# Kernel tuning notes

Measured on AMD Instinct MI355X. Metric: run time of the kernel, lower is better.

## Reference

```python
import jax, jax.numpy as jnp
import numpy as np

N_NODES = 100000


def setup_inputs() -> dict:
    key = jax.random.key(0)
    ks = jax.random.split(key, 6)
    d_in, d_hid, d_out = 128, 128, 128
    x = jax.random.normal(ks[0], (N_NODES, d_in), dtype=jnp.float32)
    # edge_index[0] = row (destination), edge_index[1] = col (source)
    edge_index = jax.random.randint(ks[1], (2, 1000000), 0, N_NODES, dtype=jnp.int64)
    W1 = jax.random.normal(ks[2], (2 * d_in, d_hid), dtype=jnp.float32) * (1.0 / np.sqrt(2 * d_in))
    b1 = jnp.zeros((d_hid,), dtype=jnp.float32)
    W2 = jax.random.normal(ks[3], (2 * d_hid, d_out), dtype=jnp.float32) * (1.0 / np.sqrt(2 * d_hid))
    b2 = jnp.zeros((d_out,), dtype=jnp.float32)
    return {"x": x, "edge_index": edge_index, "W1": W1, "b1": b1, "W2": W2, "b2": b2}


def _mean_aggregate(x, row, col, inv_deg):
    # out[i] = (1/deg(i)) * sum_{(i,j) in E} x[j]   (cogdl MeanAggregator: row_norm + spmm)
    agg = jax.ops.segment_sum(x[col], row, num_segments=x.shape[0])  # [N, d]
    return agg * inv_deg[:, None]


def _sage_layer(x, row, col, inv_deg, W, b):
    agg = _mean_aggregate(x, row, col, inv_deg)
    h = jnp.concatenate([x, agg], axis=-1)  # [N, 2d]
    return h @ W + b


def reference(x, edge_index, W1, b1, W2, b2):
    row, col = edge_index[0], edge_index[1]
    n = x.shape[0]
    deg = jax.ops.segment_sum(jnp.ones(row.shape, dtype=x.dtype), row, num_segments=n)
    inv_deg = jnp.where(deg > 0, 1.0 / jnp.maximum(deg, 1.0), 0.0).astype(x.dtype)
    h = jax.nn.relu(_sage_layer(x, row, col, inv_deg, W1, b1))
    # (dropout omitted: deterministic/eval reference)
    out = _sage_layer(h, row, col, inv_deg, W2, b2)
    return out
```

## Files before the change

### kernel.cpp

```cpp
#include <hip/hip_runtime.h>

#define D 128
#define MAXDEG 64
#define BIN_SHIFT 7
#define BINCAP 2048
#define EPB 8192

typedef short short8 __attribute__((ext_vector_type(8)));
typedef short short4v __attribute__((ext_vector_type(4)));
typedef float float4v __attribute__((ext_vector_type(4)));

__device__ __forceinline__ unsigned short f2bf(float f) {
    union { float f; unsigned u; } v; v.f = f;
    unsigned r = v.u + 0x7FFFu + ((v.u >> 16) & 1u);
    return (unsigned short)(r >> 16);
}
__device__ __forceinline__ float bflo(unsigned p) {
    union { unsigned u; float f; } v; v.u = p << 16; return v.f;
}
__device__ __forceinline__ float bfhi(unsigned p) {
    union { unsigned u; float f; } v; v.u = p & 0xFFFF0000u; return v.f;
}

__global__ __launch_bounds__(1024) void bin_kernel(const int* __restrict__ row,
                                                   const int* __restrict__ col,
                                                   int* __restrict__ bincnt,
                                                   long long* __restrict__ binbuf,
                                                   int nE, int nbins) {
    __shared__ int bcnt[1024];
    __shared__ int bbase[1024];
    const int t = threadIdx.x;
    const int e0 = blockIdx.x * EPB + t * 8;
    if (t < nbins) bcnt[t] = 0;
    __syncthreads();

    int rr[8], cc[8], bin[8], pos[8];
    if (e0 + 8 <= nE) {
        int4 r0 = *(const int4*)&row[e0];
        int4 r1 = *(const int4*)&row[e0 + 4];
        int4 c0 = *(const int4*)&col[e0];
        int4 c1 = *(const int4*)&col[e0 + 4];
        rr[0] = r0.x; rr[1] = r0.y; rr[2] = r0.z; rr[3] = r0.w;
        rr[4] = r1.x; rr[5] = r1.y; rr[6] = r1.z; rr[7] = r1.w;
        cc[0] = c0.x; cc[1] = c0.y; cc[2] = c0.z; cc[3] = c0.w;
        cc[4] = c1.x; cc[5] = c1.y; cc[6] = c1.z; cc[7] = c1.w;
        #pragma unroll
        for (int k = 0; k < 8; ++k) {
            bin[k] = rr[k] >> BIN_SHIFT;
            pos[k] = atomicAdd(&bcnt[bin[k]], 1);
        }
    } else {
        #pragma unroll
        for (int k = 0; k < 8; ++k) {
            int e = e0 + k;
            if (e < nE) {
                rr[k] = row[e]; cc[k] = col[e];
                bin[k] = rr[k] >> BIN_SHIFT;
                pos[k] = atomicAdd(&bcnt[bin[k]], 1);
            } else { pos[k] = -1; bin[k] = 0; rr[k] = 0; cc[k] = 0; }
        }
    }
    __syncthreads();

    if (t < nbins) {
        int c = bcnt[t];
        bbase[t] = (c > 0) ? atomicAdd(&bincnt[t << 4], c) : 0;
    }
    __syncthreads();

    #pragma unroll
    for (int k = 0; k < 8; ++k) {
        if (pos[k] >= 0) {
            int slot = bbase[bin[k]] + pos[k];
            if (slot < BINCAP)
                binbuf[(size_t)bin[k] * BINCAP + slot] =
                    ((long long)cc[k] << 32) | (unsigned)rr[k];
        }
    }
}

__global__ __launch_bounds__(256) void ellbuild_kernel(const long long* __restrict__ binbuf,
                                                       const int* __restrict__ bincnt,
                                                       int* __restrict__ cnt,
                                                       int* __restrict__ bucket, int n) {
    __shared__ int lcnt[1 << BIN_SHIFT];
    const int b = blockIdx.x, t = threadIdx.x;
    const int base = b << BIN_SHIFT;
    if (t < (1 << BIN_SHIFT)) lcnt[t] = 0;
    __syncthreads();
    int m = bincnt[b << 4];
    if (m > BINCAP) m = BINCAP;
    const long long* buf = binbuf + (size_t)b * BINCAP;
    for (int j = t; j < m; j += 256) {
        long long pk = buf[j];
        int r = (int)pk;
        int c = (int)(pk >> 32);
        int pos = atomicAdd(&lcnt[r - base], 1);
        if (pos < MAXDEG) bucket[((size_t)r << 6) + pos] = c;
    }
    __syncthreads();
    if (t < (1 << BIN_SHIFT)) {
        int node = base + t;
        if (node < n) {
            int c0 = lcnt[t];
            cnt[node] = c0;
            int c = c0 > MAXDEG ? MAXDEG : c0;
            int cp = (c + 15) & ~15;
            for (int s = c; s < cp; ++s) bucket[((size_t)node << 6) + s] = n;
        }
    }
}

__global__ void conv_kernel(const float2* __restrict__ x, unsigned* __restrict__ xb, int nPairs,
                            const float* __restrict__ W1, const float* __restrict__ W2,
                            unsigned short* __restrict__ Wt1, unsigned short* __restrict__ Wt2,
                            unsigned* __restrict__ hb, int n) {
    int id = blockIdx.x * blockDim.x + threadIdx.x;
    if (blockIdx.x < 256) {
        int e = id & 32767;
        int c = e >> 8, k = e & 255;
        if (id < 32768) Wt1[c * 256 + k] = f2bf(W1[k * 128 + c]);
        else            Wt2[c * 256 + k] = f2bf(W2[k * 128 + c]);
    } else {
        if (blockIdx.x == 256 && threadIdx.x < 64) {
            xb[((size_t)n << 6) + threadIdx.x] = 0;
            hb[((size_t)n << 6) + threadIdx.x] = 0;
        }
        int stride = (gridDim.x - 256) * blockDim.x;
        for (int i = id - 65536; i < nPairs; i += stride) {
            float2 v = x[i];
            xb[i] = (unsigned)f2bf(v.x) | ((unsigned)f2bf(v.y) << 16);
        }
    }
}

__device__ __forceinline__ void gather16(const unsigned* __restrict__ feat,
                                         const int* __restrict__ bk, int j, unsigned lane,
                                         float& x0, float& x1, float& x2, float& x3,
                                         float& y0, float& y1, float& y2, float& y3) {
    int4 c0 = *(const int4*)&bk[j];
    int4 c1 = *(const int4*)&bk[j + 4];
    int4 c2 = *(const int4*)&bk[j + 8];
    int4 c3 = *(const int4*)&bk[j + 12];
    unsigned v0  = feat[((unsigned)c0.x << 6) + lane];
    unsigned v1  = feat[((unsigned)c0.y << 6) + lane];
    unsigned v2  = feat[((unsigned)c0.z << 6) + lane];
    unsigned v3  = feat[((unsigned)c0.w << 6) + lane];
    unsigned v4  = feat[((unsigned)c1.x << 6) + lane];
    unsigned v5  = feat[((unsigned)c1.y << 6) + lane];
    unsigned v6  = feat[((unsigned)c1.z << 6) + lane];
    unsigned v7  = feat[((unsigned)c1.w << 6) + lane];
    unsigned v8  = feat[((unsigned)c2.x << 6) + lane];
    unsigned v9  = feat[((unsigned)c2.y << 6) + lane];
    unsigned v10 = feat[((unsigned)c2.z << 6) + lane];
    unsigned v11 = feat[((unsigned)c2.w << 6) + lane];
    unsigned v12 = feat[((unsigned)c3.x << 6) + lane];
    unsigned v13 = feat[((unsigned)c3.y << 6) + lane];
    unsigned v14 = feat[((unsigned)c3.z << 6) + lane];
    unsigned v15 = feat[((unsigned)c3.w << 6) + lane];
    x0 += bflo(v0);  y0 += bfhi(v0);
    x1 += bflo(v1);  y1 += bfhi(v1);
    x2 += bflo(v2);  y2 += bfhi(v2);
    x3 += bflo(v3);  y3 += bfhi(v3);
    x0 += bflo(v4);  y0 += bfhi(v4);
    x1 += bflo(v5);  y1 += bfhi(v5);
    x2 += bflo(v6);  y2 += bfhi(v6);
    x3 += bflo(v7);  y3 += bfhi(v7);
    x0 += bflo(v8);  y0 += bfhi(v8);
    x1 += bflo(v9);  y1 += bfhi(v9);
    x2 += bflo(v10); y2 += bfhi(v10);
    x3 += bflo(v11); y3 += bfhi(v11);
    x0 += bflo(v12); y0 += bfhi(v12);
    x1 += bflo(v13); y1 += bfhi(v13);
    x2 += bflo(v14); y2 += bfhi(v14);
    x3 += bflo(v15); y3 += bfhi(v15);
}

__global__ __launch_bounds__(256) void agg_bf16_kernel(const unsigned* __restrict__ feat,
                                                       const int* __restrict__ cnt,
                                                       const int* __restrict__ bucket,
                                                       unsigned* __restrict__ agg, int n) {
    long long tid = (long long)blockIdx.x * blockDim.x + threadIdx.x;
    int w = (int)(tid >> 6);
    int iA = w * 2, iB = w * 2 + 1;
    if (iA >= n) return;
    const unsigned lane = (unsigned)tid & 63u;

    int dtA = cnt[iA];
    int dA = dtA > MAXDEG ? MAXDEG : dtA;
    int dpA = (dA + 15) & ~15;
    int dtB = 0, dpB = 0;
    if (iB < n) {
        dtB = cnt[iB];
        int dB = dtB > MAXDEG ? MAXDEG : dtB;
        dpB = (dB + 15) & ~15;
    }
    const int* bkA = bucket + ((size_t)iA << 6);
    const int* bkB = bucket + ((size_t)iB << 6);

    float ax0=0,ax1=0,ax2=0,ax3=0, ay0=0,ay1=0,ay2=0,ay3=0;
    float bx0=0,bx1=0,bx2=0,bx3=0, by0=0,by1=0,by2=0,by3=0;
    int jm = dpA > dpB ? dpA : dpB;
    for (int j = 0; j < jm; j += 16) {
        if (j < dpA) gather16(feat, bkA, j, lane, ax0,ax1,ax2,ax3, ay0,ay1,ay2,ay3);
        if (j < dpB) gather16(feat, bkB, j, lane, bx0,bx1,bx2,bx3, by0,by1,by2,by3);
    }

    float invA = (dtA > 0) ? 1.0f / (float)dtA : 0.0f;
    float rxA = ((ax0 + ax1) + (ax2 + ax3)) * invA;
    float ryA = ((ay0 + ay1) + (ay2 + ay3)) * invA;
    agg[((size_t)iA << 6) + lane] = (unsigned)f2bf(rxA) | ((unsigned)f2bf(ryA) << 16);
    if (iB < n) {
        float invB = (dtB > 0) ? 1.0f / (float)dtB : 0.0f;
        float rxB = ((bx0 + bx1) + (bx2 + bx3)) * invB;
        float ryB = ((by0 + by1) + (by2 + by3)) * invB;
        agg[((size_t)iB << 6) + lane] = (unsigned)f2bf(rxB) | ((unsigned)f2bf(ryB) << 16);
    }
}

template <bool RELU, bool OUTF32>
__global__ __launch_bounds__(256) void sage_mfma(const unsigned short* __restrict__ selfb,
                                                 const unsigned short* __restrict__ aggb,
                                                 const unsigned short* __restrict__ Wtb,
                                                 const float* __restrict__ bias,
                                                 float* __restrict__ outf,
                                                 unsigned short* __restrict__ outb,
                                                 int n) {
    __shared__ short Alds[64 * 256];
    const int tid  = threadIdx.x;
    const int wave = tid >> 6;
    const int lane = tid & 63;
    const int r15  = lane & 15, g = lane >> 4;
    const int rowbase = blockIdx.x * 64;

    #pragma unroll
    for (int it = 0; it < 8; ++it) {
        int id  = it * 256 + tid;
        int row = id >> 5, cin = id & 31;
        int rowG = rowbase + row; if (rowG >= n) rowG = n - 1;
        const unsigned short* src = (cin < 16)
            ? selfb + (size_t)rowG * D + cin * 8
            : aggb  + (size_t)rowG * D + (cin - 16) * 8;
        int dchunk = cin ^ (row & 7);
        *(short8*)&Alds[row * 256 + dchunk * 8] = *(const short8*)src;
    }

    const int colbase = wave * 32;
    short8 bfr[2][8];
    #pragma unroll
    for (int cf = 0; cf < 2; ++cf) {
        const unsigned short* wp = Wtb + (size_t)(colbase + cf * 16 + r15) * 256;
        #pragma unroll
        for (int ks = 0; ks < 8; ++ks) {
            short4v lo = *(const short4v*)(wp + ks * 32 + 4 * g);
            short4v hi = *(const short4v*)(wp + ks * 32 + 16 + 4 * g);
            bfr[cf][ks] = __builtin_shufflevector(lo, hi, 0, 1, 2, 3, 4, 5, 6, 7);
        }
    }
    float bv0 = bias[colbase + r15];
    float bv1 = bias[colbase + 16 + r15];
    float4v acc[4][2];
    #pragma unroll
    for (int rf = 0; rf < 4; ++rf) {
        acc[rf][0] = (float4v){bv0, bv0, bv0, bv0};
        acc[rf][1] = (float4v){bv1, bv1, bv1, bv1};
    }

    __syncthreads();

    const int sw = (r15 & 7) << 4;
    #pragma unroll
    for (int ks = 0; ks < 8; ++ks) {
        #pragma unroll
        for (int rf = 0; rf < 4; ++rf) {
            const char* pr = (const char*)&Alds[(rf * 16 + r15) * 256];
            short4v lo = *(const short4v*)(pr + ((ks * 64 + 8 * g) ^ sw));
            short4v hi = *(const short4v*)(pr + ((ks * 64 + 8 * g + 32) ^ sw));
            short8 af = __builtin_shufflevector(lo, hi, 0, 1, 2, 3, 4, 5, 6, 7);
            acc[rf][0] = __builtin_amdgcn_mfma_f32_16x16x32_bf16(af, bfr[0][ks], acc[rf][0], 0, 0, 0);
            acc[rf][1] = __builtin_amdgcn_mfma_f32_16x16x32_bf16(af, bfr[1][ks], acc[rf][1], 0, 0, 0);
        }
    }

    #pragma unroll
    for (int rf = 0; rf < 4; ++rf) {
        #pragma unroll
        for (int cf = 0; cf < 2; ++cf) {
            #pragma unroll
            for (int r = 0; r < 4; ++r) {
                int row = rowbase + rf * 16 + g * 4 + r;
                int col = colbase + cf * 16 + r15;
                if (row < n) {
                    float v = acc[rf][cf][r];
                    if (RELU) v = (v > 0.0f) ? v : 0.0f;
                    if (OUTF32) outf[(size_t)row * D + col] = v;
                    else        outb[(size_t)row * D + col] = f2bf(v);
                }
            }
        }
    }
}

extern "C" void kernel_launch(void* const* d_in, const int* in_sizes, int n_in,
                              void* d_out, int out_size, void* d_ws, size_t ws_size,
                              hipStream_t stream) {
    const float* x  = (const float*)d_in[0];
    const int*   ei = (const int*)d_in[1];
    const float* W1 = (const float*)d_in[2];
    const float* b1 = (const float*)d_in[3];
    const float* W2 = (const float*)d_in[4];
    const float* b2 = (const float*)d_in[5];
    float* out = (float*)d_out;

    const int n  = in_sizes[0] / D;
    const int nE = in_sizes[1] / 2;
    const int* row = ei;
    const int* col = ei + nE;
    const int nbins = (n + (1 << BIN_SHIFT) - 1) >> BIN_SHIFT;

    auto aup = [](size_t v) { return (v + 63) & ~(size_t)63; };
    int* wsI = (int*)d_ws;
    size_t o = 0;
    int* cnt    = wsI + o; o = aup(o + (size_t)n);
    int* bucket = wsI + o; o = aup(o + ((size_t)n << 6));
    unsigned* xb   = (unsigned*)(wsI + o); o = aup(o + (size_t)(n + 1) * 64);
    unsigned* hb   = (unsigned*)(wsI + o); o = aup(o + (size_t)(n + 1) * 64);
    unsigned* aggb = (unsigned*)(wsI + o); o = aup(o + (size_t)n * 64);
    unsigned short* Wt1 = (unsigned short*)(wsI + o); o = aup(o + 16384);
    unsigned short* Wt2 = (unsigned short*)(wsI + o); o = aup(o + 16384);
    int* bincnt = wsI + o; o = aup(o + (size_t)nbins * 16);
    long long* binbuf = (long long*)aggb;

    const int B = 256;
    const int binGrid = (nE + EPB - 1) / EPB;
    const int aggGrid = (int)((((long long)(n + 1) / 2) * 64 + B - 1) / B);
    const int mmGrid  = (n + 63) / 64;

    hipMemsetAsync(bincnt, 0, (size_t)nbins * 16 * sizeof(int), stream);
    bin_kernel<<<binGrid, 1024, 0, stream>>>(row, col, bincnt, binbuf, nE, nbins);
    ellbuild_kernel<<<nbins, B, 0, stream>>>(binbuf, bincnt, cnt, bucket, n);

    conv_kernel<<<2048 + 256, B, 0, stream>>>((const float2*)x, xb, n * 64,
                                              W1, W2, Wt1, Wt2, hb, n);

    agg_bf16_kernel<<<aggGrid, B, 0, stream>>>(xb, cnt, bucket, aggb, n);
    sage_mfma<true, false><<<mmGrid, B, 0, stream>>>(
        (const unsigned short*)xb, (const unsigned short*)aggb, Wt1, b1,
        nullptr, (unsigned short*)hb, n);

    agg_bf16_kernel<<<aggGrid, B, 0, stream>>>(hb, cnt, bucket, aggb, n);
    sage_mfma<false, true><<<mmGrid, B, 0, stream>>>(
        (const unsigned short*)hb, (const unsigned short*)aggb, Wt2, b2,
        out, nullptr, n);
}
```

Measured before the change: 200.8 us.

## Merge binning and conversion kernels; shrink GEMM row tile and stream weight fragments

Folds the edge-binning kernel and the bf16 conversion/weight-transpose kernel into one launch, with block ranges assigned to each task, to save a launch and let the two independent phases overlap. The MFMA linear-layer kernel now handles 32 rows per block instead of 64, which halves LDS use and doubles the block count. It also double-buffers B fragments from global memory per k-step instead of preloading all of them into registers. Per-block weight reloads grow, and the smaller tile gives less reuse of each weight fragment.

```diff
diff --git a/kernel.cpp b/kernel.cpp
--- a/kernel.cpp
+++ b/kernel.cpp
@@ -22,59 +22,87 @@
     union { unsigned u; float f; } v; v.u = p & 0xFFFF0000u; return v.f;
 }
 
-__global__ __launch_bounds__(1024) void bin_kernel(const int* __restrict__ row,
-                                                   const int* __restrict__ col,
-                                                   int* __restrict__ bincnt,
-                                                   long long* __restrict__ binbuf,
-                                                   int nE, int nbins) {
+__global__ __launch_bounds__(1024) void prep_kernel(const int* __restrict__ row,
+                                                    const int* __restrict__ col,
+                                                    int* __restrict__ bincnt,
+                                                    long long* __restrict__ binbuf,
+                                                    int nE, int nbins, int binGrid,
+                                                    const float2* __restrict__ x,
+                                                    unsigned* __restrict__ xb, int nPairs,
+                                                    const float* __restrict__ W1,
+                                                    const float* __restrict__ W2,
+                                                    unsigned short* __restrict__ Wt1,
+                                                    unsigned short* __restrict__ Wt2,
+                                                    unsigned* __restrict__ hb, int n) {
     __shared__ int bcnt[1024];
     __shared__ int bbase[1024];
     const int t = threadIdx.x;
-    const int e0 = blockIdx.x * EPB + t * 8;
-    if (t < nbins) bcnt[t] = 0;
-    __syncthreads();
-
-    int rr[8], cc[8], bin[8], pos[8];
-    if (e0 + 8 <= nE) {
-        int4 r0 = *(const int4*)&row[e0];
-        int4 r1 = *(const int4*)&row[e0 + 4];
-        int4 c0 = *(const int4*)&col[e0];
-        int4 c1 = *(const int4*)&col[e0 + 4];
-        rr[0] = r0.x; rr[1] = r0.y; rr[2] = r0.z; rr[3] = r0.w;
-        rr[4] = r1.x; rr[5] = r1.y; rr[6] = r1.z; rr[7] = r1.w;
-        cc[0] = c0.x; cc[1] = c0.y; cc[2] = c0.z; cc[3] = c0.w;
-        cc[4] = c1.x; cc[5] = c1.y; cc[6] = c1.z; cc[7] = c1.w;
+
+    if (blockIdx.x < (unsigned)binGrid) {
+        const int e0 = blockIdx.x * EPB + t * 8;
+        if (t < nbins) bcnt[t] = 0;
+        __syncthreads();
+
+        int rr[8], cc[8], bin[8], pos[8];
+        if (e0 + 8 <= nE) {
+            int4 r0 = *(const int4*)&row[e0];
+            int4 r1 = *(const int4*)&row[e0 + 4];
+            int4 c0 = *(const int4*)&col[e0];
+            int4 c1 = *(const int4*)&col[e0 + 4];
+            rr[0] = r0.x; rr[1] = r0.y; rr[2] = r0.z; rr[3] = r0.w;
+            rr[4] = r1.x; rr[5] = r1.y; rr[6] = r1.z; rr[7] = r1.w;
+            cc[0] = c0.x; cc[1] = c0.y; cc[2] = c0.z; cc[3] = c0.w;
+            cc[4] = c1.x; cc[5] = c1.y; cc[6] = c1.z; cc[7] = c1.w;
+            #pragma unroll
+            for (int k = 0; k < 8; ++k) {
+                bin[k] = rr[k] >> BIN_SHIFT;
+                pos[k] = atomicAdd(&bcnt[bin[k]], 1);
+            }
+        } else {
+            #pragma unroll
+            for (int k = 0; k < 8; ++k) {
+                int e = e0 + k;
+                if (e < nE) {
+                    rr[k] = row[e]; cc[k] = col[e];
+                    bin[k] = rr[k] >> BIN_SHIFT;
+                    pos[k] = atomicAdd(&bcnt[bin[k]], 1);
+                } else { pos[k] = -1; bin[k] = 0; rr[k] = 0; cc[k] = 0; }
+            }
+        }
+        __syncthreads();
+
+        if (t < nbins) {
+            int c = bcnt[t];
+            bbase[t] = (c > 0) ? atomicAdd(&bincnt[t << 4], c) : 0;
+        }
+        __syncthreads();
+
         #pragma unroll
         for (int k = 0; k < 8; ++k) {
-            bin[k] = rr[k] >> BIN_SHIFT;
-            pos[k] = atomicAdd(&bcnt[bin[k]], 1);
-        }
+            if (pos[k] >= 0) {
+                int slot = bbase[bin[k]] + pos[k];
+                if (slot < BINCAP)
+                    binbuf[(size_t)bin[k] * BINCAP + slot] =
+                        ((long long)cc[k] << 32) | (unsigned)rr[k];
+            }
+        }
+    } else if (blockIdx.x < (unsigned)(binGrid + 64)) {
+        int id = (blockIdx.x - binGrid) * 1024 + t;
+        int e = id & 32767;
+        int c = e >> 8, k = e & 255;
+        if (id < 32768) Wt1[c * 256 + k] = f2bf(W1[k * 128 + c]);
+        else            Wt2[c * 256 + k] = f2bf(W2[k * 128 + c]);
     } else {
-        #pragma unroll
-        for (int k = 0; k < 8; ++k) {
-            int e = e0 + k;
-            if (e < nE) {
-                rr[k] = row[e]; cc[k] = col[e];
-                bin[k] = rr[k] >> BIN_SHIFT;
-                pos[k] = atomicAdd(&bcnt[bin[k]], 1);
-            } else { pos[k] = -1; bin[k] = 0; rr[k] = 0; cc[k] = 0; }
-        }
-    }
-    __syncthreads();
-
-    if (t < nbins) {
-        int c = bcnt[t];
-        bbase[t] = (c > 0) ? atomicAdd(&bincnt[t << 4], c) : 0;
-    }
-    __syncthreads();
-
-    #pragma unroll
-    for (int k = 0; k < 8; ++k) {
-        if (pos[k] >= 0) {
-            int slot = bbase[bin[k]] + pos[k];
-            if (slot < BINCAP)
-                binbuf[(size_t)bin[k] * BINCAP + slot] =
-                    ((long long)cc[k] << 32) | (unsigned)rr[k];
+        int cb = blockIdx.x - binGrid - 64;
+        if (cb == 0 && t < 64) {
+            xb[((size_t)n << 6) + t] = 0;
+            hb[((size_t)n << 6) + t] = 0;
+        }
+        int id = cb * 1024 + t;
+        int stride = (gridDim.x - binGrid - 64) * 1024;
+        for (int i = id; i < nPairs; i += stride) {
+            float2 v = x[i];
+            xb[i] = (unsigned)f2bf(v.x) | ((unsigned)f2bf(v.y) << 16);
         }
     }
 }
@@ -107,29 +135,6 @@
             int c = c0 > MAXDEG ? MAXDEG : c0;
             int cp = (c + 15) & ~15;
             for (int s = c; s < cp; ++s) bucket[((size_t)node << 6) + s] = n;
-        }
-    }
-}
-
-__global__ void conv_kernel(const float2* __restrict__ x, unsigned* __restrict__ xb, int nPairs,
-                            const float* __restrict__ W1, const float* __restrict__ W2,
-                            unsigned short* __restrict__ Wt1, unsigned short* __restrict__ Wt2,
-                            unsigned* __restrict__ hb, int n) {
-    int id = blockIdx.x * blockDim.x + threadIdx.x;
-    if (blockIdx.x < 256) {
-        int e = id & 32767;
-        int c = e >> 8, k = e & 255;
-        if (id < 32768) Wt1[c * 256 + k] = f2bf(W1[k * 128 + c]);
-        else            Wt2[c * 256 + k] = f2bf(W2[k * 128 + c]);
-    } else {
-        if (blockIdx.x == 256 && threadIdx.x < 64) {
-            xb[((size_t)n << 6) + threadIdx.x] = 0;
-            hb[((size_t)n << 6) + threadIdx.x] = 0;
-        }
-        int stride = (gridDim.x - 256) * blockDim.x;
-        for (int i = id - 65536; i < nPairs; i += stride) {
-            float2 v = x[i];
-            xb[i] = (unsigned)f2bf(v.x) | ((unsigned)f2bf(v.y) << 16);
         }
     }
 }
@@ -218,6 +223,12 @@
     }
 }
 
+__device__ __forceinline__ short8 loadB(const unsigned short* __restrict__ wp, int ks, int g) {
+    short4v lo = *(const short4v*)(wp + ks * 32 + 4 * g);
+    short4v hi = *(const short4v*)(wp + ks * 32 + 16 + 4 * g);
+    return __builtin_shufflevector(lo, hi, 0, 1, 2, 3, 4, 5, 6, 7);
+}
+
 template <bool RELU, bool OUTF32>
 __global__ __launch_bounds__(256) void sage_mfma(const unsigned short* __restrict__ selfb,
                                                  const unsigned short* __restrict__ aggb,
@@ -226,15 +237,15 @@
                                                  float* __restrict__ outf,
                                                  unsigned short* __restrict__ outb,
                                                  int n) {
-    __shared__ short Alds[64 * 256];
+    __shared__ short Alds[32 * 256];
     const int tid  = threadIdx.x;
     const int wave = tid >> 6;
     const int lane = tid & 63;
     const int r15  = lane & 15, g = lane >> 4;
-    const int rowbase = blockIdx.x * 64;
+    const int rowbase = blockIdx.x * 32;
 
     #pragma unroll
-    for (int it = 0; it < 8; ++it) {
+    for (int it = 0; it < 4; ++it) {
         int id  = it * 256 + tid;
         int row = id >> 5, cin = id & 31;
         int rowG = rowbase + row; if (rowG >= n) rowG = n - 1;
@@ -246,44 +257,45 @@
     }
 
     const int colbase = wave * 32;
-    short8 bfr[2][8];
-    #pragma unroll
-    for (int cf = 0; cf < 2; ++cf) {
-        const unsigned short* wp = Wtb + (size_t)(colbase + cf * 16 + r15) * 256;
-        #pragma unroll
-        for (int ks = 0; ks < 8; ++ks) {
-            short4v lo = *(const short4v*)(wp + ks * 32 + 4 * g);
-            short4v hi = *(const short4v*)(wp + ks * 32 + 16 + 4 * g);
-            bfr[cf][ks] = __builtin_shufflevector(lo, hi, 0, 1, 2, 3, 4, 5, 6, 7);
-        }
-    }
+    const unsigned short* wp0 = Wtb + (size_t)(colbase + r15) * 256;
+    const unsigned short* wp1 = Wtb + (size_t)(colbase + 16 + r15) * 256;
     float bv0 = bias[colbase + r15];
     float bv1 = bias[colbase + 16 + r15];
-    float4v acc[4][2];
+    float4v acc[2][2];
     #pragma unroll
-    for (int rf = 0; rf < 4; ++rf) {
+    for (int rf = 0; rf < 2; ++rf) {
         acc[rf][0] = (float4v){bv0, bv0, bv0, bv0};
         acc[rf][1] = (float4v){bv1, bv1, bv1, bv1};
     }
+
+    short8 b0a = loadB(wp0, 0, g), b1a = loadB(wp1, 0, g);
+    short8 b0b = loadB(wp0, 1, g), b1b = loadB(wp1, 1, g);
 
     __syncthreads();
 
     const int sw = (r15 & 7) << 4;
     #pragma unroll
     for (int ks = 0; ks < 8; ++ks) {
+        short8 cur0, cur1;
+        if (ks & 1) { cur0 = b0b; cur1 = b1b; }
+        else        { cur0 = b0a; cur1 = b1a; }
+        if (ks < 6) {
+            if (ks & 1) { b0b = loadB(wp0, ks + 2, g); b1b = loadB(wp1, ks + 2, g); }
+            else        { b0a = loadB(wp0, ks + 2, g); b1a = loadB(wp1, ks + 2, g); }
+        }
         #pragma unroll
-        for (int rf = 0; rf < 4; ++rf) {
+        for (int rf = 0; rf < 2; ++rf) {
             const char* pr = (const char*)&Alds[(rf * 16 + r15) * 256];
             short4v lo = *(const short4v*)(pr + ((ks * 64 + 8 * g) ^ sw));
             short4v hi = *(const short4v*)(pr + ((ks * 64 + 8 * g + 32) ^ sw));
             short8 af = __builtin_shufflevector(lo, hi, 0, 1, 2, 3, 4, 5, 6, 7);
-            acc[rf][0] = __builtin_amdgcn_mfma_f32_16x16x32_bf16(af, bfr[0][ks], acc[rf][0], 0, 0, 0);
-            acc[rf][1] = __builtin_amdgcn_mfma_f32_16x16x32_bf16(af, bfr[1][ks], acc[rf][1], 0, 0, 0);
+            acc[rf][0] = __builtin_amdgcn_mfma_f32_16x16x32_bf16(af, cur0, acc[rf][0], 0, 0, 0);
+            acc[rf][1] = __builtin_amdgcn_mfma_f32_16x16x32_bf16(af, cur1, acc[rf][1], 0, 0, 0);
         }
     }
 
     #pragma unroll
-    for (int rf = 0; rf < 4; ++rf) {
+    for (int rf = 0; rf < 2; ++rf) {
         #pragma unroll
         for (int cf = 0; cf < 2; ++cf) {
             #pragma unroll
@@ -334,14 +346,13 @@
     const int B = 256;
     const int binGrid = (nE + EPB - 1) / EPB;
     const int aggGrid = (int)((((long long)(n + 1) / 2) * 64 + B - 1) / B);
-    const int mmGrid  = (n + 63) / 64;
+    const int mmGrid  = (n + 31) / 32;
 
     hipMemsetAsync(bincnt, 0, (size_t)nbins * 16 * sizeof(int), stream);
-    bin_kernel<<<binGrid, 1024, 0, stream>>>(row, col, bincnt, binbuf, nE, nbins);
+    prep_kernel<<<binGrid + 64 + 512, 1024, 0, stream>>>(
+        row, col, bincnt, binbuf, nE, nbins, binGrid,
+        (const float2*)x, xb, n * 64, W1, W2, Wt1, Wt2, hb, n);
     ellbuild_kernel<<<nbins, B, 0, stream>>>(binbuf, bincnt, cnt, bucket, n);
-
-    conv_kernel<<<2048 + 256, B, 0, stream>>>((const float2*)x, xb, n * 64,
-                                              W1, W2, Wt1, Wt2, hb, n);
 
     agg_bf16_kernel<<<aggGrid, B, 0, stream>>>(xb, cnt, bucket, aggb, n);
     sage_mfma<true, false><<<mmGrid, B, 0, stream>>>(
```

Measured after the change: 229.1 us. 1.14x slower.
